# Optimization experiments

Measured on AMD Instinct MI355X. Metric: run time of the kernel, lower is better.

Reference implementation:

```python
import jax, jax.numpy as jnp
import numpy as np

B, S, HID = 2, 2048, 2048
NH, NKV, D = 16, 4, 128  # heads, kv heads, dim_per_head
ROPE_BASE = 10000.0


def setup_inputs() -> dict:
    key = jax.random.key(0)
    ks = jax.random.split(key, 5)
    x = jax.random.normal(ks[0], (B, S, HID), jnp.float32)
    wq = jax.random.normal(ks[1], (HID, NH * D), jnp.float32) * 0.02
    wk = jax.random.normal(ks[2], (HID, NKV * D), jnp.float32) * 0.02
    wv = jax.random.normal(ks[3], (HID, NKV * D), jnp.float32) * 0.02
    wo = jax.random.normal(ks[4], (NH * D, HID), jnp.float32) * 0.02
    inv_freq = 1.0 / (ROPE_BASE ** (jnp.arange(0, D, 2, dtype=jnp.float32) / D))
    freqs = jnp.outer(jnp.arange(S, dtype=jnp.float32), inv_freq)  # [S, D/2]
    cos, sin = jnp.cos(freqs), jnp.sin(freqs)
    mask = jnp.tril(jnp.ones((S, S), dtype=bool))  # causal, True = attend
    return {"x": x, "wq": wq, "wk": wk, "wv": wv, "wo": wo,
            "cos": cos, "sin": sin, "mask": mask}


def _rope_interleave(t, cos, sin):
    # t: [B, H, S, D]; cos/sin: [S, D/2]; interleaved pairs (even, odd)
    te, to = t[..., ::2], t[..., 1::2]
    c, s = cos[None, None], sin[None, None]
    re = te * c - to * s
    ro = to * c + te * s
    return jnp.stack([re, ro], axis=-1).reshape(t.shape)


def reference(x, wq, wk, wv, wo, cos, sin, mask):
    b, s, _ = x.shape
    # QKV projections + shape(): [B, S, hid] -> [B, H, S, D]
    q = (x @ wq).reshape(b, s, NH, D).transpose(0, 2, 1, 3)
    k = (x @ wk).reshape(b, s, NKV, D).transpose(0, 2, 1, 3)
    v = (x @ wv).reshape(b, s, NKV, D).transpose(0, 2, 1, 3)
    q = _rope_interleave(q, cos, sin)
    k = _rope_interleave(k, cos, sin)
    # GQA: repeat each kv head heads//heads_kv times consecutively
    rep = NH // NKV
    k = jnp.repeat(k, rep, axis=1)
    v = jnp.repeat(v, rep, axis=1)
    scores = jnp.einsum('bhqd,bhkd->bhqk', q, k) * (D ** -0.5)
    scores = scores.astype(jnp.float32)
    scores = jnp.where(mask[None, None], scores, jnp.finfo(jnp.float32).min)
    attn = jax.nn.softmax(scores, axis=-1).astype(x.dtype)
    ctx = jnp.einsum('bhqk,bhkd->bhqd', attn, v)
    ctx = ctx.transpose(0, 2, 1, 3).reshape(b, s, NH * D)  # unshape()
    return ctx @ wo
```

## Files before the change

kernel.cpp:

```cpp
#include <hip/hip_runtime.h>
#include <hip/hip_bf16.h>
#include <math.h>

#define S_LEN 2048
#define HIDW 2048
#define NHEAD 16
#define NKVH 4
#define HD 128
#define NB 2
#define MROWS (NB * S_LEN)
#define QKVN (NHEAD * HD + 2 * NKVH * HD)
#define KOFF (NHEAD * HD)
#define VOFF (NHEAD * HD + NKVH * HD)

typedef __bf16 bf16_t;
typedef __bf16 bf16x4_t __attribute__((ext_vector_type(4)));
typedef __bf16 bf16x8_t __attribute__((ext_vector_type(8)));
typedef float f32x4_t __attribute__((ext_vector_type(4)));

__device__ __forceinline__ void gload_lds16(const bf16_t* g, bf16_t* l) {
  __builtin_amdgcn_global_load_lds(
      (const __attribute__((address_space(1))) void*)g,
      (__attribute__((address_space(3))) void*)l, 16, 0, 0);
}

__device__ __forceinline__ f32x4_t zero4() {
  f32x4_t z = {0.f, 0.f, 0.f, 0.f};
  return z;
}

__device__ __forceinline__ float fexp2(float x) {
#if __has_builtin(__builtin_amdgcn_exp2f)
  return __builtin_amdgcn_exp2f(x);
#else
  return exp2f(x);
#endif
}

__global__ __launch_bounds__(256) void k_cvt8(const float* __restrict__ in,
                                              bf16_t* __restrict__ out, int n8) {
  int i = blockIdx.x * 256 + threadIdx.x;
  if (i >= n8) return;
  const float4* p = (const float4*)(in + (size_t)i * 8);
  float4 a = p[0], b = p[1];
  bf16x8_t r;
  r[0] = (bf16_t)a.x; r[1] = (bf16_t)a.y; r[2] = (bf16_t)a.z; r[3] = (bf16_t)a.w;
  r[4] = (bf16_t)b.x; r[5] = (bf16_t)b.y; r[6] = (bf16_t)b.z; r[7] = (bf16_t)b.w;
  *(bf16x8_t*)(out + (size_t)i * 8) = r;
}

__global__ __launch_bounds__(256) void k_tr_cvt(const float* __restrict__ in,
                                                bf16_t* __restrict__ out, int R, int C) {
  __shared__ float t[32][33];
  int c0 = blockIdx.x * 32, r0 = blockIdx.y * 32;
  int tx = threadIdx.x & 31, ty = threadIdx.x >> 5;
#pragma unroll
  for (int rr = ty; rr < 32; rr += 8) t[rr][tx] = in[(size_t)(r0 + rr) * C + c0 + tx];
  __syncthreads();
#pragma unroll
  for (int rr = ty; rr < 32; rr += 8)
    out[(size_t)(c0 + rr) * R + r0 + tx] = (bf16_t)t[tx][rr];
}

template <int EPI, int BMH>
__global__ __launch_bounds__(512, 2) void k_gemm256(const bf16_t* __restrict__ A,
                                                    const bf16_t* __restrict__ Bt,
                                                    void* __restrict__ Cout,
                                                    int M, int N, int K, int nby,
                                                    const float* __restrict__ cosT,
                                                    const float* __restrict__ sinT) {
  __shared__ bf16_t As[2][BMH * 128 * 64];
  __shared__ bf16_t Bs[2][256 * 64];

  int tid = threadIdx.x;
  int lane = tid & 63, wid = tid >> 6;
  int l15 = lane & 15, lg = lane >> 4;
  int wrb = (wid >> 2) * (BMH * 64);
  int wcb = (wid & 3) * 64;

  int nwg = gridDim.x;
  int qx = nwg >> 3;
  int lin = blockIdx.x;
  int wg = (lin & 7) * qx + (lin >> 3);
  int row0 = (wg / nby) * (BMH * 128), col0 = (wg % nby) * 256;

  int srow = tid >> 3;
  int scol = ((tid & 7) ^ (srow & 7)) * 8;
  const bf16_t* Ag = A + (size_t)(row0 + srow) * K + scol;
  const bf16_t* Bg = Bt + (size_t)(col0 + srow) * K + scol;

  f32x4_t acc[BMH * 4][4];
#pragma unroll
  for (int i = 0; i < BMH * 4; i++)
#pragma unroll
    for (int j = 0; j < 4; j++) acc[i][j] = zero4();

  int xr = (l15 & 7) << 4;

#pragma unroll
  for (int u = 0; u < BMH * 2; u++)
    gload_lds16(Ag + (size_t)u * 64 * K, As[0] + u * 4096 + tid * 8);
#pragma unroll
  for (int u = 0; u < 4; u++)
    gload_lds16(Bg + (size_t)u * 64 * K, Bs[0] + u * 4096 + tid * 8);
  asm volatile("s_waitcnt vmcnt(0)" ::: "memory");
  __builtin_amdgcn_s_barrier();
  __builtin_amdgcn_sched_barrier(0);

  int nk = K >> 6;
  for (int t = 0; t < nk; t++) {
    int cur = t & 1;
    const char* Ac = (const char*)As[cur];
    const char* Bc = (const char*)Bs[cur];
    bf16_t* An = As[cur ^ 1];
    bf16_t* Bn = Bs[cur ^ 1];
    const bf16_t* Agn = Ag + (size_t)(t + 1) * 64;
    const bf16_t* Bgn = Bg + (size_t)(t + 1) * 64;
    bool pf = (t + 1 < nk);

    bf16x8_t af[4][2];
#pragma unroll
    for (int ph = 0; ph < 4; ph++) {
      const int mh = (BMH == 2) ? (ph >> 1) : 0;
      const int nh = (BMH == 2) ? (ph & 1) : ph;
      const int NJ = (BMH == 2) ? 2 : 1;
      if ((BMH == 2) ? (nh == 0) : (ph == 0)) {
#pragma unroll
        for (int i = 0; i < 4; i++) {
          int row = wrb + (mh * 4 + i) * 16 + l15;
#pragma unroll
          for (int kk = 0; kk < 2; kk++)
            af[i][kk] = *(const bf16x8_t*)(Ac + ((row * 128 + kk * 64 + lg * 16) ^ xr));
        }
      }
      bf16x8_t bfr[NJ][2];
#pragma unroll
      for (int j = 0; j < NJ; j++) {
        int rowb = wcb + (nh * NJ + j) * 16 + l15;
#pragma unroll
        for (int kk = 0; kk < 2; kk++)
          bfr[j][kk] = *(const bf16x8_t*)(Bc + ((rowb * 128 + kk * 64 + lg * 16) ^ xr));
      }
      if (pf) {
        if (BMH == 2) {
          if (ph == 0) {
            gload_lds16(Agn, An + tid * 8);
            gload_lds16(Agn + (size_t)64 * K, An + 4096 + tid * 8);
            gload_lds16(Bgn, Bn + tid * 8);
          } else if (ph == 1) {
            gload_lds16(Agn + (size_t)128 * K, An + 8192 + tid * 8);
            gload_lds16(Agn + (size_t)192 * K, An + 12288 + tid * 8);
            gload_lds16(Bgn + (size_t)64 * K, Bn + 4096 + tid * 8);
          } else if (ph == 2) {
            gload_lds16(Bgn + (size_t)128 * K, Bn + 8192 + tid * 8);
            gload_lds16(Bgn + (size_t)192 * K, Bn + 12288 + tid * 8);
          }
        } else {
          if (ph == 0) {
            gload_lds16(Agn, An + tid * 8);
            gload_lds16(Agn + (size_t)64 * K, An + 4096 + tid * 8);
          } else if (ph == 1) {
            gload_lds16(Bgn, Bn + tid * 8);
            gload_lds16(Bgn + (size_t)64 * K, Bn + 4096 + tid * 8);
          } else if (ph == 2) {
            gload_lds16(Bgn + (size_t)128 * K, Bn + 8192 + tid * 8);
            gload_lds16(Bgn + (size_t)192 * K, Bn + 12288 + tid * 8);
          }
        }
      }
      __builtin_amdgcn_s_barrier();
      __builtin_amdgcn_s_setprio(1);
#pragma unroll
      for (int i = 0; i < 4; i++)
#pragma unroll
        for (int j = 0; j < NJ; j++)
#pragma unroll
          for (int kk = 0; kk < 2; kk++)
            acc[mh * 4 + i][nh * NJ + j] = __builtin_amdgcn_mfma_f32_16x16x32_bf16(
                af[i][kk], bfr[j][kk], acc[mh * 4 + i][nh * NJ + j], 0, 0, 0);
      __builtin_amdgcn_s_setprio(0);
      if (ph < 3) __builtin_amdgcn_s_barrier();
    }
    if (pf) asm volatile("s_waitcnt vmcnt(0)" ::: "memory");
    __builtin_amdgcn_s_barrier();
    __builtin_amdgcn_sched_barrier(0);
  }

  if (EPI == 2) {
    if (col0 < VOFF) {
      int sbase = row0 & (S_LEN - 1);
      bf16_t* cosL = &As[0][0];
      bf16_t* sinL = &Bs[0][0];
#pragma unroll
      for (int k = 0; k < 8; k++) {
        gload_lds16((const bf16_t*)(cosT + (size_t)sbase * 64 + k * 2048 + tid * 4),
                    cosL + k * 4096 + tid * 8);
        gload_lds16((const bf16_t*)(sinT + (size_t)sbase * 64 + k * 2048 + tid * 4),
                    sinL + k * 4096 + tid * 8);
      }
      asm volatile("s_waitcnt vmcnt(0)" ::: "memory");
      __builtin_amdgcn_s_barrier();
      const float* cosF = (const float*)cosL;
      const float* sinF = (const float*)sinL;
      const float QS = 0.08838834764831845f * 1.4426950408889634f;
#pragma unroll
      for (int i = 0; i < BMH * 4; i++) {
#pragma unroll
        for (int j = 0; j < 4; j++) {
          int c = col0 + wcb + j * 16 + l15;
          int rlb = wrb + i * 16 + lg * 4;
          float scale = (c < KOFF) ? QS : 1.0f;
          int p0 = (c & 127) >> 1;
          int codd = c & 1;
#pragma unroll
          for (int qd = 0; qd < 4; qd++) {
            int rl = rlb + qd;
            float self = acc[i][j][qd];
            float other = __shfl_xor(self, 1);
            float cv = cosF[rl * 64 + p0], sv = sinF[rl * 64 + p0];
            float outv = codd ? (self * cv + other * sv) : (self * cv - other * sv);
            ((bf16_t*)Cout)[(size_t)(row0 + rl) * N + c] = (bf16_t)(outv * scale);
          }
        }
      }
    } else {
#pragma unroll
      for (int i = 0; i < BMH * 4; i++) {
#pragma unroll
        for (int j = 0; j < 4; j++) {
          int r = row0 + wrb + i * 16 + lg * 4;
          int c = col0 + wcb + j * 16 + l15;
#pragma unroll
          for (int qd = 0; qd < 4; qd++)
            ((bf16_t*)Cout)[(size_t)(r + qd) * N + c] = (bf16_t)acc[i][j][qd];
        }
      }
    }
  } else {
#pragma unroll
    for (int i = 0; i < BMH * 4; i++) {
#pragma unroll
      for (int j = 0; j < 4; j++) {
        int r = row0 + wrb + i * 16 + lg * 4;
        int c = col0 + wcb + j * 16 + l15;
#pragma unroll
        for (int qd = 0; qd < 4; qd++)
          ((float*)Cout)[(size_t)(r + qd) * N + c] = acc[i][j][qd];
      }
    }
  }
}

__global__ __launch_bounds__(256) void k_vt(const bf16_t* __restrict__ qkv,
                                            bf16_t* __restrict__ vt) {
  __shared__ bf16_t t[32][33];
  int s0 = blockIdx.x * 32;
  int dt = (blockIdx.y & 3) * 32;
  int h = blockIdx.y >> 2;
  int b = blockIdx.z;
  int tx = threadIdx.x & 31, ty = threadIdx.x >> 5;
#pragma unroll
  for (int rr = ty; rr < 32; rr += 8)
    t[rr][tx] = qkv[(size_t)(b * S_LEN + s0 + rr) * QKVN + VOFF + h * HD + dt + tx];
  __syncthreads();
#pragma unroll
  for (int rr = ty; rr < 32; rr += 8)
    vt[((size_t)((b * NKVH + h) * HD + dt + rr)) * S_LEN + s0 + tx] = t[tx][rr];
}

__global__ __launch_bounds__(256, 2) void k_attn(const bf16_t* __restrict__ qkv,
                                                 const bf16_t* __restrict__ vt,
                                                 bf16_t* __restrict__ ctx) {
  __shared__ bf16_t Ks[2 * 64 * 128];
  __shared__ bf16_t Vs[2 * 128 * 64];
  __shared__ bf16_t plds[4][16 * 72];

  int tid = threadIdx.x;
  int lane = tid & 63, wid = tid >> 6;
  int idx = blockIdx.x;
  int bh = idx & 31;
  int qg = 31 - (idx >> 5);
  int b = bh >> 4, h = bh & 15;
  int kvh = h >> 2;
  int q0 = qg * 64 + wid * 16;
  int l15 = lane & 15, lg = lane >> 4;

  const bf16_t* Kbase = qkv + (size_t)(b * S_LEN) * QKVN + KOFF + kvh * HD;
  const bf16_t* Vbase = vt + (size_t)(b * NKVH + kvh) * HD * S_LEN;

  const bf16_t* Qp = qkv + (size_t)(b * S_LEN + q0 + l15) * QKVN + h * HD + lg * 8;
  bf16x8_t aq[4];
#pragma unroll
  for (int kk = 0; kk < 4; kk++) aq[kk] = *(const bf16x8_t*)(Qp + kk * 32);

  int Ls[4], Lk[4], Lv[4];
#pragma unroll
  for (int u = 0; u < 4; u++) {
    int L = u * 4096 + tid * 16;
    Ls[u] = L >> 1;
    Lk[u] = L ^ (((L >> 8) & 7) << 4);
    Lv[u] = L ^ (((L >> 7) & 7) << 4);
  }

  f32x4_t o[8];
#pragma unroll
  for (int j = 0; j < 8; j++) o[j] = zero4();
  float ms = -INFINITY, lsum = 0.f;

  bf16_t* pbuf = &plds[wid][0];
  int xr = (l15 & 7) << 4;
  int ntiles = qg + 1;
  int qcol = q0 + l15;

#pragma unroll
  for (int u = 0; u < 4; u++) {
    gload_lds16(Kbase + (size_t)(Lk[u] >> 8) * QKVN + ((Lk[u] & 255) >> 1), Ks + Ls[u]);
    gload_lds16(Vbase + (size_t)(Lv[u] >> 7) * S_LEN + ((Lv[u] & 127) >> 1), Vs + Ls[u]);
  }
  __syncthreads();

  for (int t = 0; t < ntiles; t++) {
    int kv0 = t * 64;
    if (t + 1 < ntiles) {
      const bf16_t* Kn = Kbase + (size_t)(kv0 + 64) * QKVN;
      const bf16_t* Vn = Vbase + kv0 + 64;
      int bo = ((t + 1) & 1) * 8192;
#pragma unroll
      for (int u = 0; u < 4; u++) {
        gload_lds16(Kn + (size_t)(Lk[u] >> 8) * QKVN + ((Lk[u] & 255) >> 1), Ks + bo + Ls[u]);
        gload_lds16(Vn + (size_t)(Lv[u] >> 7) * S_LEN + ((Lv[u] & 127) >> 1), Vs + bo + Ls[u]);
      }
    }
    const char* Kb = (const char*)Ks + (t & 1) * 16384;
    const char* Vb = (const char*)Vs + (t & 1) * 16384;

    f32x4_t sacc[4];
#pragma unroll
    for (int cg = 0; cg < 4; cg++) sacc[cg] = zero4();
#pragma unroll
    for (int cg = 0; cg < 4; cg++) {
#pragma unroll
      for (int kk = 0; kk < 4; kk++) {
        int boff = ((cg * 16 + l15) * 256 + kk * 64 + lg * 16) ^ xr;
        bf16x8_t bk = *(const bf16x8_t*)(Kb + boff);
        sacc[cg] = __builtin_amdgcn_mfma_f32_16x16x32_bf16(bk, aq[kk], sacc[cg], 0, 0, 0);
      }
    }
    if (kv0 + 63 > q0) {
#pragma unroll
      for (int cg = 0; cg < 4; cg++) {
#pragma unroll
        for (int i = 0; i < 4; i++) {
          int kvg = kv0 + cg * 16 + lg * 4 + i;
          if (kvg > qcol) sacc[cg][i] = -1e30f;
        }
      }
    }
    float pmax = sacc[0][0];
#pragma unroll
    for (int cg = 0; cg < 4; cg++)
#pragma unroll
      for (int i = 0; i < 4; i++) pmax = fmaxf(pmax, sacc[cg][i]);
    pmax = fmaxf(pmax, __shfl_xor(pmax, 16));
    pmax = fmaxf(pmax, __shfl_xor(pmax, 32));
    if (__any(pmax - ms > 8.0f)) {
      float nm = fmaxf(ms, pmax);
      float sc = fexp2(ms - nm);
      ms = nm;
      lsum *= sc;
      float sci[4];
#pragma unroll
      for (int i = 0; i < 4; i++) sci[i] = __shfl(sc, lg * 4 + i);
#pragma unroll
      for (int j = 0; j < 8; j++)
#pragma unroll
        for (int i = 0; i < 4; i++) o[j][i] *= sci[i];
    }
    float ls = 0.f;
#pragma unroll
    for (int cg = 0; cg < 4; cg++)
#pragma unroll
      for (int i = 0; i < 4; i++) {
        sacc[cg][i] = fexp2(sacc[cg][i] - ms);
        ls += sacc[cg][i];
      }
    ls += __shfl_xor(ls, 16);
    ls += __shfl_xor(ls, 32);
    lsum += ls;
#pragma unroll
    for (int cg = 0; cg < 4; cg++)
#pragma unroll
      for (int i = 0; i < 4; i++)
        pbuf[l15 * 72 + cg * 16 + lg * 4 + i] = (bf16_t)sacc[cg][i];
    __builtin_amdgcn_wave_barrier();
    bf16x8_t pa0 = *(const bf16x8_t*)(pbuf + l15 * 72 + lg * 8);
    bf16x8_t pa1 = *(const bf16x8_t*)(pbuf + l15 * 72 + 32 + lg * 8);
    __builtin_amdgcn_wave_barrier();
#pragma unroll
    for (int j = 0; j < 8; j++) {
      int d = j * 16 + l15;
      int bo0 = (d * 128 + lg * 16) ^ xr;
      int bo1 = (d * 128 + 64 + lg * 16) ^ xr;
      o[j] = __builtin_amdgcn_mfma_f32_16x16x32_bf16(
          pa0, *(const bf16x8_t*)(Vb + bo0), o[j], 0, 0, 0);
      o[j] = __builtin_amdgcn_mfma_f32_16x16x32_bf16(
          pa1, *(const bf16x8_t*)(Vb + bo1), o[j], 0, 0, 0);
    }
    __syncthreads();
  }

  bf16_t* Cp = ctx + (size_t)(b * S_LEN + q0) * KOFF + h * HD;
#pragma unroll
  for (int i = 0; i < 4; i++) {
    float inv = 1.f / __shfl(lsum, lg * 4 + i);
    int row = lg * 4 + i;
#pragma unroll
    for (int j = 0; j < 8; j++)
      Cp[(size_t)row * KOFF + j * 16 + l15] = (bf16_t)(o[j][i] * inv);
  }
}

extern "C" void kernel_launch(void* const* d_in, const int* in_sizes, int n_in,
                              void* d_out, int out_size, void* d_ws, size_t ws_size,
                              hipStream_t stream) {
  const float* x = (const float*)d_in[0];
  const float* wq = (const float*)d_in[1];
  const float* wk = (const float*)d_in[2];
  const float* wv = (const float*)d_in[3];
  const float* wo = (const float*)d_in[4];
  const float* cosT = (const float*)d_in[5];
  const float* sinT = (const float*)d_in[6];

  bf16_t* xb = (bf16_t*)d_ws;
  bf16_t* wqkvT = xb + (size_t)MROWS * HIDW;
  bf16_t* woT = wqkvT + (size_t)QKVN * HIDW;
  bf16_t* qkv = woT + (size_t)HIDW * HIDW;
  bf16_t* vtb = qkv + (size_t)MROWS * QKVN;

  k_cvt8<<<MROWS * HIDW / 8 / 256, 256, 0, stream>>>(x, xb, MROWS * HIDW / 8);
  k_tr_cvt<<<dim3(KOFF / 32, HIDW / 32), 256, 0, stream>>>(wq, wqkvT, HIDW, KOFF);
  k_tr_cvt<<<dim3((NKVH * HD) / 32, HIDW / 32), 256, 0, stream>>>(
      wk, wqkvT + (size_t)KOFF * HIDW, HIDW, NKVH * HD);
  k_tr_cvt<<<dim3((NKVH * HD) / 32, HIDW / 32), 256, 0, stream>>>(
      wv, wqkvT + (size_t)VOFF * HIDW, HIDW, NKVH * HD);
  k_tr_cvt<<<dim3(HIDW / 32, KOFF / 32), 256, 0, stream>>>(wo, woT, KOFF, HIDW);
  k_gemm256<2, 2><<<(MROWS / 256) * (QKVN / 256), 512, 0, stream>>>(
      xb, wqkvT, qkv, MROWS, QKVN, HIDW, QKVN / 256, cosT, sinT);
  k_vt<<<dim3(S_LEN / 32, 4 * NKVH, NB), 256, 0, stream>>>(qkv, vtb);
  k_attn<<<32 * 32, 256, 0, stream>>>(qkv, vtb, xb);
  k_gemm256<0, 1><<<(MROWS / 128) * (HIDW / 256), 512, 0, stream>>>(
      xb, woT, d_out, MROWS, HIDW, KOFF, HIDW / 256, nullptr, nullptr);
}
```

Measured before the change: 213.8 us.

## Deepen GEMM global-to-LDS prefetch to two tiles ahead with partial vmcnt waits

The GEMM main loop now issues global-to-LDS loads for tile t+2 into the same LDS buffer being consumed. It staggers those stores across the four MFMA phases, after the corresponding A and B fragments have been read into registers. It replaces the full vmcnt(0) wait per iteration with partial waits, so one tile of loads stays in flight. All B fragments and the first A half are loaded up front, which raises register pressure. Correctness depends on the carefully ordered reads, barriers and overwrites within the shared buffer.

```diff
diff --git a/kernel.cpp b/kernel.cpp
--- a/kernel.cpp
+++ b/kernel.cpp
@@ -96,92 +96,163 @@
     for (int j = 0; j < 4; j++) acc[i][j] = zero4();
 
   int xr = (l15 & 7) << 4;
-
-#pragma unroll
-  for (int u = 0; u < BMH * 2; u++)
-    gload_lds16(Ag + (size_t)u * 64 * K, As[0] + u * 4096 + tid * 8);
-#pragma unroll
-  for (int u = 0; u < 4; u++)
-    gload_lds16(Bg + (size_t)u * 64 * K, Bs[0] + u * 4096 + tid * 8);
-  asm volatile("s_waitcnt vmcnt(0)" ::: "memory");
+  int nk = K >> 6;
+
+  auto stA = [&](int tt, int u) {
+    gload_lds16(Ag + (size_t)u * 64 * K + (size_t)tt * 64,
+                As[tt & 1] + u * 4096 + tid * 8);
+  };
+  auto stB = [&](int tt, int u) {
+    gload_lds16(Bg + (size_t)u * 64 * K + (size_t)tt * 64,
+                Bs[tt & 1] + u * 4096 + tid * 8);
+  };
+
+  for (int tt = 0; tt < 2 && tt < nk; tt++) {
+    for (int u = 0; u < BMH * 2; u++) stA(tt, u);
+    for (int u = 0; u < 4; u++) stB(tt, u);
+  }
+  if (nk > 1) {
+    if constexpr (BMH == 2) asm volatile("s_waitcnt vmcnt(8)" ::: "memory");
+    else asm volatile("s_waitcnt vmcnt(6)" ::: "memory");
+  } else {
+    asm volatile("s_waitcnt vmcnt(0)" ::: "memory");
+  }
   __builtin_amdgcn_s_barrier();
   __builtin_amdgcn_sched_barrier(0);
 
-  int nk = K >> 6;
   for (int t = 0; t < nk; t++) {
     int cur = t & 1;
     const char* Ac = (const char*)As[cur];
     const char* Bc = (const char*)Bs[cur];
-    bf16_t* An = As[cur ^ 1];
-    bf16_t* Bn = Bs[cur ^ 1];
-    const bf16_t* Agn = Ag + (size_t)(t + 1) * 64;
-    const bf16_t* Bgn = Bg + (size_t)(t + 1) * 64;
-    bool pf = (t + 1 < nk);
-
-    bf16x8_t af[4][2];
-#pragma unroll
-    for (int ph = 0; ph < 4; ph++) {
-      const int mh = (BMH == 2) ? (ph >> 1) : 0;
-      const int nh = (BMH == 2) ? (ph & 1) : ph;
-      const int NJ = (BMH == 2) ? 2 : 1;
-      if ((BMH == 2) ? (nh == 0) : (ph == 0)) {
-#pragma unroll
-        for (int i = 0; i < 4; i++) {
-          int row = wrb + (mh * 4 + i) * 16 + l15;
+    bool pf = (t + 2 < nk);
+
+    bf16x8_t af0[4][2], bfr[4][2];
+#pragma unroll
+    for (int i = 0; i < 4; i++) {
+      int row = wrb + i * 16 + l15;
+#pragma unroll
+      for (int kk = 0; kk < 2; kk++)
+        af0[i][kk] = *(const bf16x8_t*)(Ac + ((row * 128 + kk * 64 + lg * 16) ^ xr));
+    }
+#pragma unroll
+    for (int jn = 0; jn < 4; jn++) {
+      int rowb = wcb + jn * 16 + l15;
+#pragma unroll
+      for (int kk = 0; kk < 2; kk++)
+        bfr[jn][kk] = *(const bf16x8_t*)(Bc + ((rowb * 128 + kk * 64 + lg * 16) ^ xr));
+    }
+    __builtin_amdgcn_s_barrier();
+    __builtin_amdgcn_s_setprio(1);
+    if constexpr (BMH == 2) {
+#pragma unroll
+      for (int i = 0; i < 4; i++)
+#pragma unroll
+        for (int j = 0; j < 2; j++)
 #pragma unroll
           for (int kk = 0; kk < 2; kk++)
-            af[i][kk] = *(const bf16x8_t*)(Ac + ((row * 128 + kk * 64 + lg * 16) ^ xr));
-        }
-      }
-      bf16x8_t bfr[NJ][2];
-#pragma unroll
-      for (int j = 0; j < NJ; j++) {
-        int rowb = wcb + (nh * NJ + j) * 16 + l15;
+            acc[i][j] = __builtin_amdgcn_mfma_f32_16x16x32_bf16(af0[i][kk], bfr[j][kk],
+                                                                acc[i][j], 0, 0, 0);
+    } else {
+#pragma unroll
+      for (int i = 0; i < 4; i++)
 #pragma unroll
         for (int kk = 0; kk < 2; kk++)
-          bfr[j][kk] = *(const bf16x8_t*)(Bc + ((rowb * 128 + kk * 64 + lg * 16) ^ xr));
-      }
+          acc[i][0] = __builtin_amdgcn_mfma_f32_16x16x32_bf16(af0[i][kk], bfr[0][kk],
+                                                              acc[i][0], 0, 0, 0);
+    }
+    __builtin_amdgcn_s_setprio(0);
+
+    if (pf) {
+      stA(t + 2, 0);
+      if constexpr (BMH == 2) stA(t + 2, 2);
+      else stA(t + 2, 1);
+    }
+    __builtin_amdgcn_s_barrier();
+    __builtin_amdgcn_s_setprio(1);
+    if constexpr (BMH == 2) {
+#pragma unroll
+      for (int i = 0; i < 4; i++)
+#pragma unroll
+        for (int j = 0; j < 2; j++)
+#pragma unroll
+          for (int kk = 0; kk < 2; kk++)
+            acc[i][2 + j] = __builtin_amdgcn_mfma_f32_16x16x32_bf16(
+                af0[i][kk], bfr[2 + j][kk], acc[i][2 + j], 0, 0, 0);
+    } else {
+#pragma unroll
+      for (int i = 0; i < 4; i++)
+#pragma unroll
+        for (int kk = 0; kk < 2; kk++)
+          acc[i][1] = __builtin_amdgcn_mfma_f32_16x16x32_bf16(af0[i][kk], bfr[1][kk],
+                                                              acc[i][1], 0, 0, 0);
+    }
+    __builtin_amdgcn_s_setprio(0);
+
+    bf16x8_t af1[4][2];
+    if constexpr (BMH == 2) {
+#pragma unroll
+      for (int i = 0; i < 4; i++) {
+        int row = wrb + 64 + i * 16 + l15;
+#pragma unroll
+        for (int kk = 0; kk < 2; kk++)
+          af1[i][kk] = *(const bf16x8_t*)(Ac + ((row * 128 + kk * 64 + lg * 16) ^ xr));
+      }
+    }
+    if (pf) { stB(t + 2, 0); stB(t + 2, 1); }
+    __builtin_amdgcn_s_barrier();
+    __builtin_amdgcn_s_setprio(1);
+    if constexpr (BMH == 2) {
+#pragma unroll
+      for (int i = 0; i < 4; i++)
+#pragma unroll
+        for (int j = 0; j < 2; j++)
+#pragma unroll
+          for (int kk = 0; kk < 2; kk++)
+            acc[4 + i][j] = __builtin_amdgcn_mfma_f32_16x16x32_bf16(
+                af1[i][kk], bfr[j][kk], acc[4 + i][j], 0, 0, 0);
+    } else {
+#pragma unroll
+      for (int i = 0; i < 4; i++)
+#pragma unroll
+        for (int kk = 0; kk < 2; kk++)
+          acc[i][2] = __builtin_amdgcn_mfma_f32_16x16x32_bf16(af0[i][kk], bfr[2][kk],
+                                                              acc[i][2], 0, 0, 0);
+    }
+    __builtin_amdgcn_s_setprio(0);
+
+    if (pf) {
+      stB(t + 2, 2); stB(t + 2, 3);
+      if constexpr (BMH == 2) { stA(t + 2, 1); stA(t + 2, 3); }
+    }
+    __builtin_amdgcn_s_barrier();
+    __builtin_amdgcn_s_setprio(1);
+    if constexpr (BMH == 2) {
+#pragma unroll
+      for (int i = 0; i < 4; i++)
+#pragma unroll
+        for (int j = 0; j < 2; j++)
+#pragma unroll
+          for (int kk = 0; kk < 2; kk++)
+            acc[4 + i][2 + j] = __builtin_amdgcn_mfma_f32_16x16x32_bf16(
+                af1[i][kk], bfr[2 + j][kk], acc[4 + i][2 + j], 0, 0, 0);
+    } else {
+#pragma unroll
+      for (int i = 0; i < 4; i++)
+#pragma unroll
+        for (int kk = 0; kk < 2; kk++)
+          acc[i][3] = __builtin_amdgcn_mfma_f32_16x16x32_bf16(af0[i][kk], bfr[3][kk],
+                                                              acc[i][3], 0, 0, 0);
+    }
+    __builtin_amdgcn_s_setprio(0);
+
+    if (t + 1 < nk) {
       if (pf) {
-        if (BMH == 2) {
-          if (ph == 0) {
-            gload_lds16(Agn, An + tid * 8);
-            gload_lds16(Agn + (size_t)64 * K, An + 4096 + tid * 8);
-            gload_lds16(Bgn, Bn + tid * 8);
-          } else if (ph == 1) {
-            gload_lds16(Agn + (size_t)128 * K, An + 8192 + tid * 8);
-            gload_lds16(Agn + (size_t)192 * K, An + 12288 + tid * 8);
-            gload_lds16(Bgn + (size_t)64 * K, Bn + 4096 + tid * 8);
-          } else if (ph == 2) {
-            gload_lds16(Bgn + (size_t)128 * K, Bn + 8192 + tid * 8);
-            gload_lds16(Bgn + (size_t)192 * K, Bn + 12288 + tid * 8);
-          }
-        } else {
-          if (ph == 0) {
-            gload_lds16(Agn, An + tid * 8);
-            gload_lds16(Agn + (size_t)64 * K, An + 4096 + tid * 8);
-          } else if (ph == 1) {
-            gload_lds16(Bgn, Bn + tid * 8);
-            gload_lds16(Bgn + (size_t)64 * K, Bn + 4096 + tid * 8);
-          } else if (ph == 2) {
-            gload_lds16(Bgn + (size_t)128 * K, Bn + 8192 + tid * 8);
-            gload_lds16(Bgn + (size_t)192 * K, Bn + 12288 + tid * 8);
-          }
-        }
-      }
-      __builtin_amdgcn_s_barrier();
-      __builtin_amdgcn_s_setprio(1);
-#pragma unroll
-      for (int i = 0; i < 4; i++)
-#pragma unroll
-        for (int j = 0; j < NJ; j++)
-#pragma unroll
-          for (int kk = 0; kk < 2; kk++)
-            acc[mh * 4 + i][nh * NJ + j] = __builtin_amdgcn_mfma_f32_16x16x32_bf16(
-                af[i][kk], bfr[j][kk], acc[mh * 4 + i][nh * NJ + j], 0, 0, 0);
-      __builtin_amdgcn_s_setprio(0);
-      if (ph < 3) __builtin_amdgcn_s_barrier();
-    }
-    if (pf) asm volatile("s_waitcnt vmcnt(0)" ::: "memory");
+        if constexpr (BMH == 2) asm volatile("s_waitcnt vmcnt(8)" ::: "memory");
+        else asm volatile("s_waitcnt vmcnt(6)" ::: "memory");
+      } else {
+        asm volatile("s_waitcnt vmcnt(0)" ::: "memory");
+      }
+    }
     __builtin_amdgcn_s_barrier();
     __builtin_amdgcn_sched_barrier(0);
   }
```

Result: faster. 193.9 us (-9.3%).
